# Kernel tuning notes

Measured on AMD Instinct MI355X. Metric: run time of the kernel, lower is better.

## Reference

```python
import jax, jax.numpy as jnp
import numpy as np

DIM = 1024
E = 8
TOP_K = 2
HID = int(DIM * 2.68)  # 2744


def setup_inputs() -> dict:
    key = jax.random.key(0)
    ks = jax.random.split(key, 8)
    s = 0.02
    return {
        "x": jax.random.normal(ks[0], (4, 1024, DIM), dtype=jnp.float32),
        "gate_w": jax.random.normal(ks[1], (E, DIM), dtype=jnp.float32) * s,
        "w1": jax.random.normal(ks[2], (E, HID, DIM), dtype=jnp.float32) * s,
        "w2": jax.random.normal(ks[3], (E, HID, DIM), dtype=jnp.float32) * s,
        "w3": jax.random.normal(ks[4], (E, DIM, HID), dtype=jnp.float32) * s,
        "sw1": jax.random.normal(ks[5], (HID, DIM), dtype=jnp.float32) * s,
        "sw2": jax.random.normal(ks[6], (HID, DIM), dtype=jnp.float32) * s,
        "sw3": jax.random.normal(ks[7], (DIM, HID), dtype=jnp.float32) * s,
    }


def reference(x, gate_w, w1, w2, w3, sw1, sw2, sw3):
    B, T, C = x.shape
    xf = x.reshape(-1, C)  # [S, C]
    logits = xf @ gate_w.T  # [S, E]
    rw = jax.nn.softmax(logits.astype(jnp.float32), axis=-1)
    tkw, tki = jax.lax.top_k(rw, TOP_K)  # [S, K]
    nE = rw.shape[-1]
    importance = rw.mean(0)  # [E]
    load = jax.nn.one_hot(tki[:, 0], nE, dtype=jnp.float32).mean(0)  # [E]
    aux_loss = nE * (importance * load).sum()
    tkw = tkw / tkw.sum(-1, keepdims=True)
    tkw = tkw.astype(x.dtype)
    # dense all-expert SwiGLU (faithful to original: every expert on every token)
    h = jax.nn.silu(jnp.einsum('sc,ehc->seh', xf, w1)) * jnp.einsum('sc,ehc->seh', xf, w2)  # [S,E,H]
    eo = jnp.einsum('seh,ech->sec', h, w3)  # [S, E, C]
    sel = jnp.take_along_axis(eo, tki[:, :, None], axis=1)  # [S, K, C]
    weighted = (sel * tkw[:, :, None]).sum(1)  # [S, C]
    shared = (jax.nn.silu(xf @ sw1.T) * (xf @ sw2.T)) @ sw3.T  # [S, C]
    y = (weighted + shared).reshape(B, T, C)
    return y, aux_loss
```

## Files before the change

kernel.cpp:

```cpp
#include <hip/hip_runtime.h>
#include <cstdio>
#include <cstdint>

#define S_TOK 4096
#define CDIM  1024
#define EXP   8
#define HRAW  2744
#define HPAD  2816
#define MAXROWS  13312
#define MAXTILES 104
#define NSLICE1  (HPAD / 128)
#define NSLICE2  (CDIM / 256)
#define G1_BLKS  (MAXTILES * NSLICE1)

typedef __attribute__((ext_vector_type(8))) short bf16x8;
typedef __attribute__((ext_vector_type(4))) float f32x4;
typedef __attribute__((ext_vector_type(4))) unsigned short us4;
typedef unsigned short us;

__device__ __forceinline__ us f2bf(float f) {
  unsigned u = __float_as_uint(f);
  u += 0x7fffu + ((u >> 16) & 1u);
  return (us)(u >> 16);
}
__device__ __forceinline__ float bf2f(us v) {
  return __uint_as_float((unsigned)v << 16);
}

__device__ __forceinline__ void gl16(const us* g, us* l) {
  __builtin_amdgcn_global_load_lds((__attribute__((address_space(1))) void*)g,
                                   (__attribute__((address_space(3))) void*)l,
                                   16, 0, 0);
}

__device__ __forceinline__ int xcd_swz(int orig, int nwg) {
  int q = nwg >> 3, r = nwg & 7;
  int x = orig & 7, idx = orig >> 3;
  return (x < r ? x * (q + 1) : r * (q + 1) + (x - r) * q) + idx;
}

#define CH_RP1  (HPAD * CDIM / 4)
#define CH_CPR  (HPAD / 4)

__device__ __forceinline__ void cvt4_rowpad(const float* __restrict__ src,
                                            us* __restrict__ dst, int idx) {
  int m = idx / CH_RP1, rem = idx - m * CH_RP1;
  int r = rem >> 8, c4 = rem & 255;
  us4 o;
  if (r < HRAW) {
    float4 v = *(const float4*)(src + ((size_t)(m * HRAW + r) * CDIM + c4 * 4));
    o.x = f2bf(v.x); o.y = f2bf(v.y); o.z = f2bf(v.z); o.w = f2bf(v.w);
  } else { o.x = 0; o.y = 0; o.z = 0; o.w = 0; }
  *(us4*)(dst + ((size_t)(m * HPAD + r) * CDIM + c4 * 4)) = o;
}

__device__ __forceinline__ void cvt4_colpad(const float* __restrict__ src,
                                            us* __restrict__ dst, int idx) {
  int r = idx / CH_CPR, c4 = idx - r * CH_CPR;
  int c = c4 * 4;
  us4 o;
  if (c < HRAW) {
    float4 v = *(const float4*)(src + (size_t)r * HRAW + c);
    o.x = f2bf(v.x); o.y = f2bf(v.y); o.z = f2bf(v.z); o.w = f2bf(v.w);
  } else { o.x = 0; o.y = 0; o.z = 0; o.w = 0; }
  *(us4*)(dst + (size_t)r * HPAD + c) = o;
}

__global__ void __launch_bounds__(256) gate_kernel(const float* __restrict__ x,
                                                   const float* __restrict__ gw,
                                                   us* __restrict__ xb,
                                                   int* __restrict__ tki,
                                                   float* __restrict__ tkw,
                                                   float* __restrict__ probs) {
  const int wv = threadIdx.x >> 6, lane = threadIdx.x & 63;
  const int s = blockIdx.x * 4 + wv;
  const float4* xs4 = (const float4*)(x + (size_t)s * CDIM);
  float acc[8] = {0, 0, 0, 0, 0, 0, 0, 0};
#pragma unroll
  for (int j = 0; j < 4; j++) {
    float4 v = xs4[lane * 4 + j];
    int c = lane * 16 + j * 4;
    us4 ov;
    ov.x = f2bf(v.x); ov.y = f2bf(v.y); ov.z = f2bf(v.z); ov.w = f2bf(v.w);
    *(us4*)(xb + (size_t)s * CDIM + c) = ov;
#pragma unroll
    for (int ee = 0; ee < 8; ee++) {
      const float* g = gw + ee * CDIM + c;
      acc[ee] += v.x * g[0] + v.y * g[1] + v.z * g[2] + v.w * g[3];
    }
  }
#pragma unroll
  for (int ee = 0; ee < 8; ee++) {
#pragma unroll
    for (int off = 32; off > 0; off >>= 1) acc[ee] += __shfl_xor(acc[ee], off, 64);
  }
  if (lane == 0) {
    float mx = acc[0];
    for (int ee = 1; ee < 8; ee++) mx = fmaxf(mx, acc[ee]);
    float p[8], sm = 0.f;
    for (int ee = 0; ee < 8; ee++) { p[ee] = expf(acc[ee] - mx); sm += p[ee]; }
    float inv = 1.f / sm;
    for (int ee = 0; ee < 8; ee++) probs[s * 8 + ee] = p[ee] * inv;
    int i0 = 0; float b0 = p[0];
    for (int ee = 1; ee < 8; ee++) if (p[ee] > b0) { b0 = p[ee]; i0 = ee; }
    int i1 = -1; float b1 = -1.f;
    for (int ee = 0; ee < 8; ee++) if (ee != i0 && p[ee] > b1) { b1 = p[ee]; i1 = ee; }
    float rw0 = b0 * inv, rw1 = b1 * inv;
    float den = 1.f / (rw0 + rw1);
    tki[2 * s] = i0; tki[2 * s + 1] = i1;
    tkw[2 * s] = rw0 * den; tkw[2 * s + 1] = rw1 * den;
  }
}

#define CVTAB_BLKS 2048
#define AB_W1   (8 * CH_RP1)
#define AB_W2   (AB_W1 + 8 * CH_RP1)
#define AB_SW1  (AB_W2 + CH_RP1)
#define AB_SW2  (AB_SW1 + CH_RP1)

__global__ void __launch_bounds__(512) cvtab_build_kernel(
    const float* __restrict__ w1, const float* __restrict__ w2,
    const float* __restrict__ sw1, const float* __restrict__ sw2,
    us* __restrict__ w1b, us* __restrict__ w2b,
    us* __restrict__ sw1b, us* __restrict__ sw2b,
    const int* __restrict__ tki, const float* __restrict__ tkw,
    const float* __restrict__ probs, int* __restrict__ meta,
    int* __restrict__ pairtok, float* __restrict__ pairw,
    int* __restrict__ invmap, int* __restrict__ tile_expert,
    float* __restrict__ aux_out) {
  if (blockIdx.x == 0) {
    const int tid = threadIdx.x, lane = tid & 63, wv = tid >> 6;
    __shared__ int s_cnt[EXP];
    __shared__ int s_amc[EXP];
    __shared__ float s_imp[EXP];
    {
      const int e = wv;
      int c_cnt = 0, c_amc = 0;
      float imp = 0.f;
      for (int s0 = 0; s0 < S_TOK; s0 += 64) {
        int s = s0 + lane;
        int i0 = tki[2 * s], i1 = tki[2 * s + 1];
        c_cnt += (i0 == e) || (i1 == e);
        c_amc += (i0 == e);
        imp += probs[s * 8 + e];
      }
#pragma unroll
      for (int off = 32; off > 0; off >>= 1) {
        c_cnt += __shfl_xor(c_cnt, off, 64);
        c_amc += __shfl_xor(c_amc, off, 64);
        imp   += __shfl_xor(imp, off, 64);
      }
      if (lane == 0) { s_cnt[e] = c_cnt; s_amc[e] = c_amc; s_imp[e] = imp; }
    }
    __syncthreads();
    int pad[EXP], start[EXP];
    int o = S_TOK;
#pragma unroll
    for (int j = 0; j < EXP; j++) {
      pad[j] = ((s_cnt[j] + 127) >> 7) << 7;
      start[j] = o;
      o += pad[j];
    }
    const int total = o;
    for (int r = tid; r < S_TOK; r += 512) { pairtok[r] = r; pairw[r] = 1.f; }
    {
      const int e = wv;
      int base = start[e];
      for (int s0 = 0; s0 < S_TOK; s0 += 64) {
        int s = s0 + lane;
        int i0 = tki[2 * s], i1 = tki[2 * s + 1];
        bool m0 = (i0 == e), m1 = (i1 == e);
        bool mm = m0 || m1;
        unsigned long long mk = __ballot(mm);
        if (mm) {
          int pos = base + __popcll(mk & ((1ull << lane) - 1ull));
          pairtok[pos] = s;
          pairw[pos] = m0 ? tkw[2 * s] : tkw[2 * s + 1];
          invmap[2 * s + (m0 ? 0 : 1)] = pos;
        }
        base += __popcll(mk);
      }
      for (int r = base + lane; r < start[e] + pad[e]; r += 64) {
        pairtok[r] = -1; pairw[r] = 0.f;
      }
    }
    if (tid < 128) {
      int ex = 8;
      if (tid >= 32) {
        int rr = tid * 128;
#pragma unroll
        for (int j = 0; j < EXP; j++)
          if (rr >= start[j] && rr < start[j] + pad[j]) ex = j;
      }
      tile_expert[tid] = ex;
    }
    if (tid == 0) {
      meta[0] = total >> 7;
      float a = 0.f;
      for (int j = 0; j < EXP; j++)
        a += (s_imp[j] * (1.f / 4096.f)) * ((float)s_amc[j] * (1.f / 4096.f));
      aux_out[0] = 8.f * a;
    }
    return;
  }
  for (int i = (blockIdx.x - 1) * 512 + threadIdx.x; i < AB_SW2;
       i += (CVTAB_BLKS - 1) * 512) {
    if (i < AB_W1)       cvt4_rowpad(w1,  w1b,  i);
    else if (i < AB_W2)  cvt4_rowpad(w2,  w2b,  i - AB_W1);
    else if (i < AB_SW1) cvt4_rowpad(sw1, sw1b, i - AB_W2);
    else                 cvt4_rowpad(sw2, sw2b, i - AB_SW1);
  }
}

#define W3CVT_BLKS 1024
#define W3_CHUNKS  (8 * CDIM * CH_CPR)
#define W3TOT      (W3_CHUNKS + CDIM * CH_CPR)

__global__ void __launch_bounds__(256, 2) gemm1_kernel(
    const us* __restrict__ xb, const us* __restrict__ w1b, const us* __restrict__ w2b,
    const us* __restrict__ sw1b, const us* __restrict__ sw2b,
    const int* __restrict__ pairtok, const int* __restrict__ tile_expert,
    const int* __restrict__ meta, us* __restrict__ h,
    const float* __restrict__ w3, const float* __restrict__ sw3,
    us* __restrict__ w3b, us* __restrict__ sw3b) {
  if (blockIdx.x >= G1_BLKS) {
    for (int i = (blockIdx.x - G1_BLKS) * 256 + threadIdx.x; i < W3TOT;
         i += W3CVT_BLKS * 256) {
      if (i < W3_CHUNKS) cvt4_colpad(w3,  w3b,  i);
      else               cvt4_colpad(sw3, sw3b, i - W3_CHUNKS);
    }
    return;
  }
  const int wgid = xcd_swz(blockIdx.x, G1_BLKS);
  const int mt = wgid % MAXTILES;
  if (mt >= meta[0]) return;
  const int n0 = (wgid / MAXTILES) * 128;
  const int e = tile_expert[mt];
  const us* B1 = (e == 8) ? sw1b : (w1b + (size_t)e * HPAD * CDIM);
  const us* B2 = (e == 8) ? sw2b : (w2b + (size_t)e * HPAD * CDIM);
  const int row0 = mt * 128;
  __shared__ __align__(16) us sA[128 * 64];
  __shared__ __align__(16) us sB1[128 * 64];
  __shared__ __align__(16) us sB2[128 * 64];
  const int tid = threadIdx.x, lane = tid & 63;
  const int wm = tid >> 7, wn = (tid >> 6) & 1;
  const int srow = tid >> 3;
  const int soct = (tid & 7) ^ (srow & 7);
  const us* gA[4];
  const us* gB1a[4];
  const us* gB2a[4];
#pragma unroll
  for (int j = 0; j < 4; j++) {
    int t = pairtok[row0 + j * 32 + srow]; if (t < 0) t = 0;
    gA[j]   = xb + (size_t)t * CDIM + soct * 8;
    gB1a[j] = B1 + (size_t)(n0 + j * 32 + srow) * CDIM + soct * 8;
    gB2a[j] = B2 + (size_t)(n0 + j * 32 + srow) * CDIM + soct * 8;
  }
  f32x4 au[4][4], av[4][4];
#pragma unroll
  for (int m = 0; m < 4; m++)
#pragma unroll
    for (int n = 0; n < 4; n++)
#pragma unroll
      for (int r = 0; r < 4; r++) { au[m][n][r] = 0.f; av[m][n][r] = 0.f; }

  const int rl = lane & 15, fo = lane >> 4;
  const int x0 = ((0 + fo) ^ (rl & 7)) << 3;
  const int x1 = ((4 + fo) ^ (rl & 7)) << 3;
  for (int k0 = 0; k0 < CDIM; k0 += 64) {
#pragma unroll
    for (int j = 0; j < 4; j++) {
      gl16(gA[j] + k0,   &sA[(j * 256 + tid) * 8]);
      gl16(gB1a[j] + k0, &sB1[(j * 256 + tid) * 8]);
      gl16(gB2a[j] + k0, &sB2[(j * 256 + tid) * 8]);
    }
    __syncthreads();
#pragma unroll
    for (int ks = 0; ks < 2; ks++) {
      const int kx = ks ? x1 : x0;
      bf16x8 a[4], b1[4], b2[4];
#pragma unroll
      for (int m = 0; m < 4; m++)
        a[m] = *(const bf16x8*)&sA[(wm * 64 + m * 16 + rl) * 64 + kx];
#pragma unroll
      for (int n = 0; n < 4; n++) {
        b1[n] = *(const bf16x8*)&sB1[(wn * 64 + n * 16 + rl) * 64 + kx];
        b2[n] = *(const bf16x8*)&sB2[(wn * 64 + n * 16 + rl) * 64 + kx];
      }
#pragma unroll
      for (int m = 0; m < 4; m++)
#pragma unroll
        for (int n = 0; n < 4; n++) {
          au[m][n] = __builtin_amdgcn_mfma_f32_16x16x32_bf16(a[m], b1[n], au[m][n], 0, 0, 0);
          av[m][n] = __builtin_amdgcn_mfma_f32_16x16x32_bf16(a[m], b2[n], av[m][n], 0, 0, 0);
        }
    }
    __syncthreads();
  }
  const int rb = (lane >> 4) * 4, cb = lane & 15;
#pragma unroll
  for (int m = 0; m < 4; m++)
#pragma unroll
    for (int n = 0; n < 4; n++)
#pragma unroll
      for (int r = 0; r < 4; r++) {
        int row = row0 + wm * 64 + m * 16 + rb + r;
        int col = n0 + wn * 64 + n * 16 + cb;
        float u = au[m][n][r], v = av[m][n][r];
        float sg = 1.f / (1.f + __expf(-u));
        h[(size_t)row * HPAD + col] = f2bf(u * sg * v);
      }
}

__global__ void __launch_bounds__(256, 2) gemm2_kernel(
    const us* __restrict__ h, const us* __restrict__ w3b, const us* __restrict__ sw3b,
    const int* __restrict__ tile_expert, const int* __restrict__ meta,
    us* __restrict__ eo) {
  const int wgid = xcd_swz(blockIdx.x, MAXTILES * NSLICE2);
  const int mt = wgid % MAXTILES;
  if (mt >= meta[0]) return;
  const int n0 = (wgid / MAXTILES) * 256;
  const int e = tile_expert[mt];
  const us* B = (e == 8) ? sw3b : (w3b + (size_t)e * CDIM * HPAD);
  const int row0 = mt * 128;
  __shared__ __align__(16) us sA[128 * 64];
  __shared__ __align__(16) us sB[256 * 64];
  const int tid = threadIdx.x, lane = tid & 63;
  const int wm = tid >> 7, wn = (tid >> 6) & 1;
  const int srow = tid >> 3;
  const int soct = (tid & 7) ^ (srow & 7);
  const us* gA[4];
  const us* gB[8];
#pragma unroll
  for (int j = 0; j < 4; j++)
    gA[j] = h + (size_t)(row0 + j * 32 + srow) * HPAD + soct * 8;
#pragma unroll
  for (int j = 0; j < 8; j++)
    gB[j] = B + (size_t)(n0 + j * 32 + srow) * HPAD + soct * 8;
  f32x4 ac[4][8];
#pragma unroll
  for (int m = 0; m < 4; m++)
#pragma unroll
    for (int n = 0; n < 8; n++)
#pragma unroll
      for (int r = 0; r < 4; r++) ac[m][n][r] = 0.f;

  const int rl = lane & 15, fo = lane >> 4;
  const int x0 = ((0 + fo) ^ (rl & 7)) << 3;
  const int x1 = ((4 + fo) ^ (rl & 7)) << 3;
  for (int k0 = 0; k0 < HPAD; k0 += 64) {
#pragma unroll
    for (int j = 0; j < 4; j++)
      gl16(gA[j] + k0, &sA[(j * 256 + tid) * 8]);
#pragma unroll
    for (int j = 0; j < 8; j++)
      gl16(gB[j] + k0, &sB[(j * 256 + tid) * 8]);
    __syncthreads();
#pragma unroll
    for (int ks = 0; ks < 2; ks++) {
      const int kx = ks ? x1 : x0;
      bf16x8 a[4], b[8];
#pragma unroll
      for (int m = 0; m < 4; m++)
        a[m] = *(const bf16x8*)&sA[(wm * 64 + m * 16 + rl) * 64 + kx];
#pragma unroll
      for (int n = 0; n < 8; n++)
        b[n] = *(const bf16x8*)&sB[(wn * 128 + n * 16 + rl) * 64 + kx];
#pragma unroll
      for (int m = 0; m < 4; m++)
#pragma unroll
        for (int n = 0; n < 8; n++)
          ac[m][n] = __builtin_amdgcn_mfma_f32_16x16x32_bf16(a[m], b[n], ac[m][n], 0, 0, 0);
    }
    __syncthreads();
  }
  const int rb = (lane >> 4) * 4, cb = lane & 15;
#pragma unroll
  for (int m = 0; m < 4; m++)
#pragma unroll
    for (int n = 0; n < 8; n++)
#pragma unroll
      for (int r = 0; r < 4; r++) {
        int row = row0 + wm * 64 + m * 16 + rb + r;
        int col = n0 + wn * 128 + n * 16 + cb;
        eo[(size_t)row * CDIM + col] = f2bf(ac[m][n][r]);
      }
}

__global__ void __launch_bounds__(256) combine_kernel(const us* __restrict__ eo,
                                                      const int* __restrict__ invmap,
                                                      const float* __restrict__ pairw,
                                                      float* __restrict__ out) {
  const int s = blockIdx.x;
  const int c = threadIdx.x * 4;
  const int j0 = invmap[2 * s], j1 = invmap[2 * s + 1];
  const float w0 = pairw[j0], w1 = pairw[j1];
  us4 a = *(const us4*)(eo + (size_t)s * CDIM + c);
  us4 b = *(const us4*)(eo + (size_t)j0 * CDIM + c);
  us4 d = *(const us4*)(eo + (size_t)j1 * CDIM + c);
  float4 o;
  o.x = bf2f(a.x) + w0 * bf2f(b.x) + w1 * bf2f(d.x);
  o.y = bf2f(a.y) + w0 * bf2f(b.y) + w1 * bf2f(d.y);
  o.z = bf2f(a.z) + w0 * bf2f(b.z) + w1 * bf2f(d.z);
  o.w = bf2f(a.w) + w0 * bf2f(b.w) + w1 * bf2f(d.w);
  *(float4*)(out + (size_t)s * CDIM + c) = o;
}

extern "C" void kernel_launch(void* const* d_in, const int* in_sizes, int n_in,
                              void* d_out, int out_size, void* d_ws, size_t ws_size,
                              hipStream_t stream) {
  const float* x   = (const float*)d_in[0];
  const float* gw  = (const float*)d_in[1];
  const float* w1  = (const float*)d_in[2];
  const float* w2  = (const float*)d_in[3];
  const float* w3  = (const float*)d_in[4];
  const float* sw1 = (const float*)d_in[5];
  const float* sw2 = (const float*)d_in[6];
  const float* sw3 = (const float*)d_in[7];
  float* out = (float*)d_out;
  char* ws = (char*)d_ws;
  size_t off = 0;
  auto take = [&](size_t bytes) -> char* {
    char* p = ws + off;
    off = (off + bytes + 255) & ~(size_t)255;
    return p;
  };
  us* xb    = (us*)take((size_t)S_TOK * CDIM * 2);
  us* w1b   = (us*)take((size_t)EXP * HPAD * CDIM * 2);
  us* w2b   = (us*)take((size_t)EXP * HPAD * CDIM * 2);
  us* w3b   = (us*)take((size_t)EXP * CDIM * HPAD * 2);
  us* sw1b  = (us*)take((size_t)HPAD * CDIM * 2);
  us* sw2b  = (us*)take((size_t)HPAD * CDIM * 2);
  us* sw3b  = (us*)take((size_t)CDIM * HPAD * 2);
  us* hbuf  = (us*)take((size_t)MAXROWS * HPAD * 2);
  us* eo    = (us*)take((size_t)MAXROWS * CDIM * 2);
  int* pairtok = (int*)take(MAXROWS * 4);
  float* pairw = (float*)take(MAXROWS * 4);
  int* invmap  = (int*)take(S_TOK * 2 * 4);
  int* tile_expert = (int*)take(128 * 4);
  int* tki = (int*)take(S_TOK * 2 * 4);
  float* tkw = (float*)take(S_TOK * 2 * 4);
  float* probs = (float*)take(S_TOK * EXP * 4);
  int* meta = (int*)take(256);
  if (off > ws_size) {
    fprintf(stderr, "MoE kernel: ws too small, need %zu got %zu\n", off, ws_size);
    return;
  }
  gate_kernel<<<S_TOK / 4, 256, 0, stream>>>(x, gw, xb, tki, tkw, probs);
  cvtab_build_kernel<<<CVTAB_BLKS, 512, 0, stream>>>(
      w1, w2, sw1, sw2, w1b, w2b, sw1b, sw2b,
      tki, tkw, probs, meta, pairtok, pairw, invmap, tile_expert,
      out + (size_t)S_TOK * CDIM);
  gemm1_kernel<<<G1_BLKS + W3CVT_BLKS, 256, 0, stream>>>(
      xb, w1b, w2b, sw1b, sw2b, pairtok, tile_expert, meta, hbuf,
      w3, sw3, w3b, sw3b);
  gemm2_kernel<<<MAXTILES * NSLICE2, 256, 0, stream>>>(
      hbuf, w3b, sw3b, tile_expert, meta, eo);
  combine_kernel<<<S_TOK, 256, 0, stream>>>(eo, invmap, pairw, out);
}
```

Before: 400.8 us.

## Merge gate with weight conversion and split routing build into its own kernel

The gating/top-k work now runs as extra blocks inside the w1/w2/sw1/sw2 bf16 conversion kernel. The routing-table build moves into a separate single-block kernel. The aim is to overlap the gate with the bandwidth-heavy weight conversion instead of running them back to back. Conversion helpers also move from 4 to 8 elements per thread, giving 16-byte bf16 stores. This adds a tiny extra launch for the build step, and the single build block still sits on the critical path.

```diff
diff --git a/kernel.cpp b/kernel.cpp
--- a/kernel.cpp
+++ b/kernel.cpp
@@ -16,6 +16,7 @@
 typedef __attribute__((ext_vector_type(8))) short bf16x8;
 typedef __attribute__((ext_vector_type(4))) float f32x4;
 typedef __attribute__((ext_vector_type(4))) unsigned short us4;
+typedef __attribute__((ext_vector_type(8))) unsigned short us8;
 typedef unsigned short us;
 
 __device__ __forceinline__ us f2bf(float f) {
@@ -39,182 +40,191 @@
   return (x < r ? x * (q + 1) : r * (q + 1) + (x - r) * q) + idx;
 }
 
-#define CH_RP1  (HPAD * CDIM / 4)
-#define CH_CPR  (HPAD / 4)
-
-__device__ __forceinline__ void cvt4_rowpad(const float* __restrict__ src,
+#define CH8_RP1  (HPAD * CDIM / 8)
+#define CH8_CPR  (HPAD / 8)
+
+__device__ __forceinline__ void cvt8_rowpad(const float* __restrict__ src,
                                             us* __restrict__ dst, int idx) {
-  int m = idx / CH_RP1, rem = idx - m * CH_RP1;
-  int r = rem >> 8, c4 = rem & 255;
-  us4 o;
+  int m = idx / CH8_RP1, rem = idx - m * CH8_RP1;
+  int r = rem >> 7, c8 = rem & 127;
+  us8 o;
   if (r < HRAW) {
-    float4 v = *(const float4*)(src + ((size_t)(m * HRAW + r) * CDIM + c4 * 4));
-    o.x = f2bf(v.x); o.y = f2bf(v.y); o.z = f2bf(v.z); o.w = f2bf(v.w);
-  } else { o.x = 0; o.y = 0; o.z = 0; o.w = 0; }
-  *(us4*)(dst + ((size_t)(m * HPAD + r) * CDIM + c4 * 4)) = o;
-}
-
-__device__ __forceinline__ void cvt4_colpad(const float* __restrict__ src,
+    const float4* p = (const float4*)(src + ((size_t)(m * HRAW + r) * CDIM + c8 * 8));
+    float4 v0 = p[0], v1 = p[1];
+    o[0] = f2bf(v0.x); o[1] = f2bf(v0.y); o[2] = f2bf(v0.z); o[3] = f2bf(v0.w);
+    o[4] = f2bf(v1.x); o[5] = f2bf(v1.y); o[6] = f2bf(v1.z); o[7] = f2bf(v1.w);
+  } else {
+    o[0] = 0; o[1] = 0; o[2] = 0; o[3] = 0; o[4] = 0; o[5] = 0; o[6] = 0; o[7] = 0;
+  }
+  *(us8*)(dst + ((size_t)(m * HPAD + r) * CDIM + c8 * 8)) = o;
+}
+
+__device__ __forceinline__ void cvt8_colpad(const float* __restrict__ src,
                                             us* __restrict__ dst, int idx) {
-  int r = idx / CH_CPR, c4 = idx - r * CH_CPR;
-  int c = c4 * 4;
-  us4 o;
+  int r = idx / CH8_CPR, c8 = idx - r * CH8_CPR;
+  int c = c8 * 8;
+  us8 o;
   if (c < HRAW) {
-    float4 v = *(const float4*)(src + (size_t)r * HRAW + c);
-    o.x = f2bf(v.x); o.y = f2bf(v.y); o.z = f2bf(v.z); o.w = f2bf(v.w);
-  } else { o.x = 0; o.y = 0; o.z = 0; o.w = 0; }
-  *(us4*)(dst + (size_t)r * HPAD + c) = o;
-}
-
-__global__ void __launch_bounds__(256) gate_kernel(const float* __restrict__ x,
-                                                   const float* __restrict__ gw,
-                                                   us* __restrict__ xb,
-                                                   int* __restrict__ tki,
-                                                   float* __restrict__ tkw,
-                                                   float* __restrict__ probs) {
-  const int wv = threadIdx.x >> 6, lane = threadIdx.x & 63;
-  const int s = blockIdx.x * 4 + wv;
-  const float4* xs4 = (const float4*)(x + (size_t)s * CDIM);
-  float acc[8] = {0, 0, 0, 0, 0, 0, 0, 0};
-#pragma unroll
-  for (int j = 0; j < 4; j++) {
-    float4 v = xs4[lane * 4 + j];
-    int c = lane * 16 + j * 4;
-    us4 ov;
-    ov.x = f2bf(v.x); ov.y = f2bf(v.y); ov.z = f2bf(v.z); ov.w = f2bf(v.w);
-    *(us4*)(xb + (size_t)s * CDIM + c) = ov;
-#pragma unroll
-    for (int ee = 0; ee < 8; ee++) {
-      const float* g = gw + ee * CDIM + c;
-      acc[ee] += v.x * g[0] + v.y * g[1] + v.z * g[2] + v.w * g[3];
-    }
-  }
-#pragma unroll
-  for (int ee = 0; ee < 8; ee++) {
-#pragma unroll
-    for (int off = 32; off > 0; off >>= 1) acc[ee] += __shfl_xor(acc[ee], off, 64);
-  }
-  if (lane == 0) {
-    float mx = acc[0];
-    for (int ee = 1; ee < 8; ee++) mx = fmaxf(mx, acc[ee]);
-    float p[8], sm = 0.f;
-    for (int ee = 0; ee < 8; ee++) { p[ee] = expf(acc[ee] - mx); sm += p[ee]; }
-    float inv = 1.f / sm;
-    for (int ee = 0; ee < 8; ee++) probs[s * 8 + ee] = p[ee] * inv;
-    int i0 = 0; float b0 = p[0];
-    for (int ee = 1; ee < 8; ee++) if (p[ee] > b0) { b0 = p[ee]; i0 = ee; }
-    int i1 = -1; float b1 = -1.f;
-    for (int ee = 0; ee < 8; ee++) if (ee != i0 && p[ee] > b1) { b1 = p[ee]; i1 = ee; }
-    float rw0 = b0 * inv, rw1 = b1 * inv;
-    float den = 1.f / (rw0 + rw1);
-    tki[2 * s] = i0; tki[2 * s + 1] = i1;
-    tkw[2 * s] = rw0 * den; tkw[2 * s + 1] = rw1 * den;
-  }
-}
-
-#define CVTAB_BLKS 2048
-#define AB_W1   (8 * CH_RP1)
-#define AB_W2   (AB_W1 + 8 * CH_RP1)
-#define AB_SW1  (AB_W2 + CH_RP1)
-#define AB_SW2  (AB_SW1 + CH_RP1)
-
-__global__ void __launch_bounds__(512) cvtab_build_kernel(
+    const float4* p = (const float4*)(src + (size_t)r * HRAW + c);
+    float4 v0 = p[0], v1 = p[1];
+    o[0] = f2bf(v0.x); o[1] = f2bf(v0.y); o[2] = f2bf(v0.z); o[3] = f2bf(v0.w);
+    o[4] = f2bf(v1.x); o[5] = f2bf(v1.y); o[6] = f2bf(v1.z); o[7] = f2bf(v1.w);
+  } else {
+    o[0] = 0; o[1] = 0; o[2] = 0; o[3] = 0; o[4] = 0; o[5] = 0; o[6] = 0; o[7] = 0;
+  }
+  *(us8*)(dst + (size_t)r * HPAD + c) = o;
+}
+
+#define GATE_BLKS 1024
+#define CVT_BLKS  2048
+#define AB8_W1   (8 * CH8_RP1)
+#define AB8_W2   (AB8_W1 + 8 * CH8_RP1)
+#define AB8_SW1  (AB8_W2 + CH8_RP1)
+#define AB8_SW2  (AB8_SW1 + CH8_RP1)
+
+__global__ void __launch_bounds__(256) cvtgate_kernel(
+    const float* __restrict__ x, const float* __restrict__ gw,
     const float* __restrict__ w1, const float* __restrict__ w2,
     const float* __restrict__ sw1, const float* __restrict__ sw2,
-    us* __restrict__ w1b, us* __restrict__ w2b,
+    us* __restrict__ xb, us* __restrict__ w1b, us* __restrict__ w2b,
     us* __restrict__ sw1b, us* __restrict__ sw2b,
-    const int* __restrict__ tki, const float* __restrict__ tkw,
-    const float* __restrict__ probs, int* __restrict__ meta,
-    int* __restrict__ pairtok, float* __restrict__ pairw,
-    int* __restrict__ invmap, int* __restrict__ tile_expert,
-    float* __restrict__ aux_out) {
-  if (blockIdx.x == 0) {
-    const int tid = threadIdx.x, lane = tid & 63, wv = tid >> 6;
-    __shared__ int s_cnt[EXP];
-    __shared__ int s_amc[EXP];
-    __shared__ float s_imp[EXP];
-    {
-      const int e = wv;
-      int c_cnt = 0, c_amc = 0;
-      float imp = 0.f;
-      for (int s0 = 0; s0 < S_TOK; s0 += 64) {
-        int s = s0 + lane;
-        int i0 = tki[2 * s], i1 = tki[2 * s + 1];
-        c_cnt += (i0 == e) || (i1 == e);
-        c_amc += (i0 == e);
-        imp += probs[s * 8 + e];
+    int* __restrict__ tki, float* __restrict__ tkw, float* __restrict__ probs) {
+  if (blockIdx.x < GATE_BLKS) {
+    const int wv = threadIdx.x >> 6, lane = threadIdx.x & 63;
+    const int s = blockIdx.x * 4 + wv;
+    const float4* xs4 = (const float4*)(x + (size_t)s * CDIM);
+    float acc[8] = {0, 0, 0, 0, 0, 0, 0, 0};
+#pragma unroll
+    for (int j = 0; j < 4; j++) {
+      float4 v = xs4[lane * 4 + j];
+      int c = lane * 16 + j * 4;
+      us4 ov;
+      ov.x = f2bf(v.x); ov.y = f2bf(v.y); ov.z = f2bf(v.z); ov.w = f2bf(v.w);
+      *(us4*)(xb + (size_t)s * CDIM + c) = ov;
+#pragma unroll
+      for (int ee = 0; ee < 8; ee++) {
+        const float* g = gw + ee * CDIM + c;
+        acc[ee] += v.x * g[0] + v.y * g[1] + v.z * g[2] + v.w * g[3];
       }
-#pragma unroll
-      for (int off = 32; off > 0; off >>= 1) {
-        c_cnt += __shfl_xor(c_cnt, off, 64);
-        c_amc += __shfl_xor(c_amc, off, 64);
-        imp   += __shfl_xor(imp, off, 64);
+    }
+#pragma unroll
+    for (int ee = 0; ee < 8; ee++) {
+#pragma unroll
+      for (int off = 32; off > 0; off >>= 1) acc[ee] += __shfl_xor(acc[ee], off, 64);
+    }
+    if (lane == 0) {
+      float mx = acc[0];
+      for (int ee = 1; ee < 8; ee++) mx = fmaxf(mx, acc[ee]);
+      float p[8], sm = 0.f;
+      for (int ee = 0; ee < 8; ee++) { p[ee] = expf(acc[ee] - mx); sm += p[ee]; }
+      float inv = 1.f / sm;
+      for (int ee = 0; ee < 8; ee++) probs[s * 8 + ee] = p[ee] * inv;
+      int i0 = 0; float b0 = p[0];
+      for (int ee = 1; ee < 8; ee++) if (p[ee] > b0) { b0 = p[ee]; i0 = ee; }
+      int i1 = -1; float b1 = -1.f;
+      for (int ee = 0; ee < 8; ee++) if (ee != i0 && p[ee] > b1) { b1 = p[ee]; i1 = ee; }
+      float rw0 = b0 * inv, rw1 = b1 * inv;
+      float den = 1.f / (rw0 + rw1);
+      tki[2 * s] = i0; tki[2 * s + 1] = i1;
+      tkw[2 * s] = rw0 * den; tkw[2 * s + 1] = rw1 * den;
+    }
+    return;
+  }
+  for (int i = (blockIdx.x - GATE_BLKS) * 256 + threadIdx.x; i < AB8_SW2;
+       i += CVT_BLKS * 256) {
+    if (i < AB8_W1)       cvt8_rowpad(w1,  w1b,  i);
+    else if (i < AB8_W2)  cvt8_rowpad(w2,  w2b,  i - AB8_W1);
+    else if (i < AB8_SW1) cvt8_rowpad(sw1, sw1b, i - AB8_W2);
+    else                  cvt8_rowpad(sw2, sw2b, i - AB8_SW1);
+  }
+}
+
+__global__ void __launch_bounds__(512) build_kernel(const int* __restrict__ tki,
+                                                    const float* __restrict__ tkw,
+                                                    const float* __restrict__ probs,
+                                                    int* __restrict__ meta,
+                                                    int* __restrict__ pairtok,
+                                                    float* __restrict__ pairw,
+                                                    int* __restrict__ invmap,
+                                                    int* __restrict__ tile_expert,
+                                                    float* __restrict__ aux_out) {
+  const int tid = threadIdx.x, lane = tid & 63, wv = tid >> 6;
+  __shared__ int s_cnt[EXP];
+  __shared__ int s_amc[EXP];
+  __shared__ float s_imp[EXP];
+  {
+    const int e = wv;
+    int c_cnt = 0, c_amc = 0;
+    float imp = 0.f;
+    for (int s0 = 0; s0 < S_TOK; s0 += 64) {
+      int s = s0 + lane;
+      int i0 = tki[2 * s], i1 = tki[2 * s + 1];
+      c_cnt += (i0 == e) || (i1 == e);
+      c_amc += (i0 == e);
+      imp += probs[s * 8 + e];
+    }
+#pragma unroll
+    for (int off = 32; off > 0; off >>= 1) {
+      c_cnt += __shfl_xor(c_cnt, off, 64);
+      c_amc += __shfl_xor(c_amc, off, 64);
+      imp   += __shfl_xor(imp, off, 64);
+    }
+    if (lane == 0) { s_cnt[e] = c_cnt; s_amc[e] = c_amc; s_imp[e] = imp; }
+  }
+  __syncthreads();
+  int pad[EXP], start[EXP];
+  int o = S_TOK;
+#pragma unroll
+  for (int j = 0; j < EXP; j++) {
+    pad[j] = ((s_cnt[j] + 127) >> 7) << 7;
+    start[j] = o;
+    o += pad[j];
+  }
+  const int total = o;
+  for (int r = tid; r < S_TOK; r += 512) { pairtok[r] = r; pairw[r] = 1.f; }
+  {
+    const int e = wv;
+    int base = start[e];
+    for (int s0 = 0; s0 < S_TOK; s0 += 64) {
+      int s = s0 + lane;
+      int i0 = tki[2 * s], i1 = tki[2 * s + 1];
+      bool m0 = (i0 == e), m1 = (i1 == e);
+      bool mm = m0 || m1;
+      unsigned long long mk = __ballot(mm);
+      if (mm) {
+        int pos = base + __popcll(mk & ((1ull << lane) - 1ull));
+        pairtok[pos] = s;
+        pairw[pos] = m0 ? tkw[2 * s] : tkw[2 * s + 1];
+        invmap[2 * s + (m0 ? 0 : 1)] = pos;
       }
-      if (lane == 0) { s_cnt[e] = c_cnt; s_amc[e] = c_amc; s_imp[e] = imp; }
-    }
-    __syncthreads();
-    int pad[EXP], start[EXP];
-    int o = S_TOK;
-#pragma unroll
-    for (int j = 0; j < EXP; j++) {
-      pad[j] = ((s_cnt[j] + 127) >> 7) << 7;
-      start[j] = o;
-      o += pad[j];
-    }
-    const int total = o;
-    for (int r = tid; r < S_TOK; r += 512) { pairtok[r] = r; pairw[r] = 1.f; }
-    {
-      const int e = wv;
-      int base = start[e];
-      for (int s0 = 0; s0 < S_TOK; s0 += 64) {
-        int s = s0 + lane;
-        int i0 = tki[2 * s], i1 = tki[2 * s + 1];
-        bool m0 = (i0 == e), m1 = (i1 == e);
-        bool mm = m0 || m1;
-        unsigned long long mk = __ballot(mm);
-        if (mm) {
-          int pos = base + __popcll(mk & ((1ull << lane) - 1ull));
-          pairtok[pos] = s;
-          pairw[pos] = m0 ? tkw[2 * s] : tkw[2 * s + 1];
-          invmap[2 * s + (m0 ? 0 : 1)] = pos;
-        }
-        base += __popcll(mk);
-      }
-      for (int r = base + lane; r < start[e] + pad[e]; r += 64) {
-        pairtok[r] = -1; pairw[r] = 0.f;
-      }
-    }
-    if (tid < 128) {
-      int ex = 8;
-      if (tid >= 32) {
-        int rr = tid * 128;
-#pragma unroll
-        for (int j = 0; j < EXP; j++)
-          if (rr >= start[j] && rr < start[j] + pad[j]) ex = j;
-      }
-      tile_expert[tid] = ex;
-    }
-    if (tid == 0) {
-      meta[0] = total >> 7;
-      float a = 0.f;
+      base += __popcll(mk);
+    }
+    for (int r = base + lane; r < start[e] + pad[e]; r += 64) {
+      pairtok[r] = -1; pairw[r] = 0.f;
+    }
+  }
+  if (tid < 128) {
+    int ex = 8;
+    if (tid >= 32) {
+      int rr = tid * 128;
+#pragma unroll
       for (int j = 0; j < EXP; j++)
-        a += (s_imp[j] * (1.f / 4096.f)) * ((float)s_amc[j] * (1.f / 4096.f));
-      aux_out[0] = 8.f * a;
-    }
-    return;
-  }
-  for (int i = (blockIdx.x - 1) * 512 + threadIdx.x; i < AB_SW2;
-       i += (CVTAB_BLKS - 1) * 512) {
-    if (i < AB_W1)       cvt4_rowpad(w1,  w1b,  i);
-    else if (i < AB_W2)  cvt4_rowpad(w2,  w2b,  i - AB_W1);
-    else if (i < AB_SW1) cvt4_rowpad(sw1, sw1b, i - AB_W2);
-    else                 cvt4_rowpad(sw2, sw2b, i - AB_SW1);
+        if (rr >= start[j] && rr < start[j] + pad[j]) ex = j;
+    }
+    tile_expert[tid] = ex;
+  }
+  if (tid == 0) {
+    meta[0] = total >> 7;
+    float a = 0.f;
+    for (int j = 0; j < EXP; j++)
+      a += (s_imp[j] * (1.f / 4096.f)) * ((float)s_amc[j] * (1.f / 4096.f));
+    aux_out[0] = 8.f * a;
   }
 }
 
 #define W3CVT_BLKS 1024
-#define W3_CHUNKS  (8 * CDIM * CH_CPR)
-#define W3TOT      (W3_CHUNKS + CDIM * CH_CPR)
+#define W38_CHUNKS (8 * CDIM * CH8_CPR)
+#define W38_TOT    (W38_CHUNKS + CDIM * CH8_CPR)
 
 __global__ void __launch_bounds__(256, 2) gemm1_kernel(
     const us* __restrict__ xb, const us* __restrict__ w1b, const us* __restrict__ w2b,
@@ -224,10 +234,10 @@
     const float* __restrict__ w3, const float* __restrict__ sw3,
     us* __restrict__ w3b, us* __restrict__ sw3b) {
   if (blockIdx.x >= G1_BLKS) {
-    for (int i = (blockIdx.x - G1_BLKS) * 256 + threadIdx.x; i < W3TOT;
+    for (int i = (blockIdx.x - G1_BLKS) * 256 + threadIdx.x; i < W38_TOT;
          i += W3CVT_BLKS * 256) {
-      if (i < W3_CHUNKS) cvt4_colpad(w3,  w3b,  i);
-      else               cvt4_colpad(sw3, sw3b, i - W3_CHUNKS);
+      if (i < W38_CHUNKS) cvt8_colpad(w3,  w3b,  i);
+      else                cvt8_colpad(sw3, sw3b, i - W38_CHUNKS);
     }
     return;
   }
@@ -446,11 +456,10 @@
     fprintf(stderr, "MoE kernel: ws too small, need %zu got %zu\n", off, ws_size);
     return;
   }
-  gate_kernel<<<S_TOK / 4, 256, 0, stream>>>(x, gw, xb, tki, tkw, probs);
-  cvtab_build_kernel<<<CVTAB_BLKS, 512, 0, stream>>>(
-      w1, w2, sw1, sw2, w1b, w2b, sw1b, sw2b,
-      tki, tkw, probs, meta, pairtok, pairw, invmap, tile_expert,
-      out + (size_t)S_TOK * CDIM);
+  cvtgate_kernel<<<GATE_BLKS + CVT_BLKS, 256, 0, stream>>>(
+      x, gw, w1, w2, sw1, sw2, xb, w1b, w2b, sw1b, sw2b, tki, tkw, probs);
+  build_kernel<<<1, 512, 0, stream>>>(tki, tkw, probs, meta, pairtok, pairw, invmap,
+                                      tile_expert, out + (size_t)S_TOK * CDIM);
   gemm1_kernel<<<G1_BLKS + W3CVT_BLKS, 256, 0, stream>>>(
       xb, w1b, w2b, sw1b, sw2b, pairtok, tile_expert, meta, hbuf,
       w3, sw3, w3b, sw3b);
```

Result: slower. 409.4 us (+2.1%).
